# Performance work log

Hardware: AMD Instinct MI355X
Metric: run time of the kernel (lower is better)

Reference implementation:

```python
import jax, jax.numpy as jnp
import numpy as np

B, T = 32, 2000
H = 512          # hidden_size
NH = 100         # n_harmonics
NM = 65          # n_magnitudes
E = 16           # energy_state dim
HH = 256         # hypernetwork hidden


def _lin_init(k, out_d, in_d):
    return jax.random.normal(k, (out_d, in_d), jnp.float32) / np.sqrt(in_d)


def setup_inputs() -> dict:
    key = jax.random.key(0)
    ks = jax.random.split(key, 24)
    inp = {
        'f0_scaled': jax.random.uniform(ks[0], (B, T), jnp.float32),
        'loudness': jax.random.uniform(ks[1], (B, T), jnp.float32),
        'energy_state': jax.random.normal(ks[2], (B, E), jnp.float32),
        # base decoder params
        'pre_W': _lin_init(ks[3], H, 2), 'pre_b': jnp.zeros((H,), jnp.float32),
        'W_ih': _lin_init(ks[4], 3 * H, H), 'W_hh': _lin_init(ks[5], 3 * H, H),
        'b_ih': jnp.zeros((3 * H,), jnp.float32), 'b_hh': jnp.zeros((3 * H,), jnp.float32),
        'post_W': _lin_init(ks[6], H, H), 'post_b': jnp.zeros((H,), jnp.float32),
        'harm_W': _lin_init(ks[7], NH, H), 'harm_b': jnp.zeros((NH,), jnp.float32),
        'noise_W': _lin_init(ks[8], NM, H), 'noise_b': jnp.zeros((NM,), jnp.float32),
        # hypernetwork params (small output scale so deltas are perturbative)
        'hyp_W1': _lin_init(ks[9], HH, E), 'hyp_b1': jnp.zeros((HH,), jnp.float32),
        'hyp_Wdh': _lin_init(ks[10], NH * H, HH) * 0.05, 'hyp_bdh': jnp.zeros((NH * H,), jnp.float32),
        'hyp_Wbh': _lin_init(ks[11], NH, HH) * 0.05, 'hyp_bbh': jnp.zeros((NH,), jnp.float32),
        'hyp_Wdn': _lin_init(ks[12], NM * H, HH) * 0.05, 'hyp_bdn': jnp.zeros((NM * H,), jnp.float32),
        'hyp_Wbn': _lin_init(ks[13], NM, HH) * 0.05, 'hyp_bbn': jnp.zeros((NM,), jnp.float32),
    }
    return inp


def _gru(x, W_ih, W_hh, b_ih, b_hh):
    # x: [B,T,H] -> [B,T,H], torch nn.GRU cell equations
    gi = jnp.einsum('bth,gh->btg', x, W_ih) + b_ih  # [B,T,3H]
    gi = jnp.swapaxes(gi, 0, 1)  # [T,B,3H]
    h0 = jnp.zeros((x.shape[0], W_hh.shape[1]), x.dtype)

    def step(h, gi_t):
        gh = h @ W_hh.T + b_hh
        ir, iz, in_ = jnp.split(gi_t, 3, axis=-1)
        hr, hz, hn = jnp.split(gh, 3, axis=-1)
        r = jax.nn.sigmoid(ir + hr)
        z = jax.nn.sigmoid(iz + hz)
        n = jnp.tanh(in_ + r * hn)
        h_new = (1.0 - z) * n + z * h
        return h_new, h_new

    _, ys = jax.lax.scan(step, h0, gi)
    return jnp.swapaxes(ys, 0, 1)  # [B,T,H]


def reference(f0_scaled, loudness, energy_state,
              pre_W, pre_b, W_ih, W_hh, b_ih, b_hh, post_W, post_b,
              harm_W, harm_b, noise_W, noise_b,
              hyp_W1, hyp_b1, hyp_Wdh, hyp_bdh, hyp_Wbh, hyp_bbh,
              hyp_Wdn, hyp_bdn, hyp_Wbn, hyp_bbn):
    Bs = energy_state.shape[0]
    # Hypernetwork: energy_state -> per-batch weight/bias deltas
    h = jax.nn.relu(energy_state @ hyp_W1.T + hyp_b1)            # [B,HH]
    dW_harm = (h @ hyp_Wdh.T + hyp_bdh).reshape(Bs, NH, H)
    db_harm = h @ hyp_Wbh.T + hyp_bbh                            # [B,NH]
    dW_noise = (h @ hyp_Wdn.T + hyp_bdn).reshape(Bs, NM, H)
    db_noise = h @ hyp_Wbn.T + hyp_bbn                           # [B,NM]

    # Base decoder trunk
    x = jnp.stack([f0_scaled, loudness], axis=-1)                # [B,T,2]
    x = jax.nn.leaky_relu(jnp.einsum('bti,hi->bth', x, pre_W) + pre_b)
    x = _gru(x, W_ih, W_hh, b_ih, b_hh)
    x = jax.nn.leaky_relu(jnp.einsum('bth,oh->bto', x, post_W) + post_b)

    # Modulated heads: per-batch effective weight shared across T (no [B*T,O,H] blow-up)
    eff_hW = harm_W[None] + dW_harm                              # [B,NH,H]
    eff_hb = harm_b[None] + db_harm                              # [B,NH]
    harm_out = jnp.einsum('bth,boh->bto', x, eff_hW) + eff_hb[:, None, :]
    harmonic_amps = jax.nn.sigmoid(harm_out)                     # [B,T,NH]

    eff_nW = noise_W[None] + dW_noise                            # [B,NM,H]
    eff_nb = noise_b[None] + db_noise                            # [B,NM]
    noise_out = jnp.einsum('bth,boh->bto', x, eff_nW) + eff_nb[:, None, :]
    noise_mags = jax.nn.sigmoid(noise_out)                       # [B,T,NM]
    return harmonic_amps, noise_mags
```

## Files before the change

kernel.cpp:

```cpp
#include <hip/hip_runtime.h>
#include <hip/hip_fp16.h>
#include <stdint.h>

#define B_  32
#define T_  2000
#define H_  512
#define NH_ 100
#define NM_ 65

typedef _Float16 f16x8 __attribute__((ext_vector_type(8)));
typedef _Float16 f16x2 __attribute__((ext_vector_type(2)));
typedef float    f32x4 __attribute__((ext_vector_type(4)));

typedef __attribute__((address_space(3))) void lds_void_t;
typedef __attribute__((address_space(1))) void glb_void_t;

__device__ __forceinline__ void gload_lds16(const void* g, void* l) {
  __builtin_amdgcn_global_load_lds((const glb_void_t*)g, (lds_void_t*)l, 16, 0, 0);
}

__device__ __forceinline__ float sigmoidf_(float x) {
  float e = __builtin_amdgcn_exp2f(-x * 1.44269504f);
  return __builtin_amdgcn_rcpf(1.0f + e);
}
__device__ __forceinline__ float tanhf_(float x) {
  float e = __builtin_amdgcn_exp2f(x * 2.88539008f);
  return 1.0f - 2.0f * __builtin_amdgcn_rcpf(e + 1.0f);
}
__device__ __forceinline__ float dot2(unsigned w, unsigned h, float acc) {
  return __builtin_amdgcn_fdot2(__builtin_bit_cast(f16x2, w),
                                __builtin_bit_cast(f16x2, h), acc, false);
}
__device__ __forceinline__ unsigned pack2(float a, float b) {
  __half2 h = __floats2half2_rn(a, b);
  return __builtin_bit_cast(unsigned, h);
}
__device__ __forceinline__ float hsel(unsigned w, int hi) {
  __half2 h2 = __builtin_bit_cast(__half2, w);
  return hi ? __high2float(h2) : __low2float(h2);
}

__global__ void hyper1(const float* __restrict__ es, const float* __restrict__ W1,
                       const float* __restrict__ b1, float* __restrict__ hE) {
  int b = blockIdx.x, o = threadIdx.x;
  float a = b1[o];
  #pragma unroll
  for (int c = 0; c < 16; ++c) a += es[b*16 + c] * W1[o*16 + c];
  hE[b*256 + o] = fmaxf(a, 0.f);
}

__global__ void hyper2(const float* __restrict__ hE,
                       const float* __restrict__ Wbh, const float* __restrict__ bbh,
                       const float* __restrict__ harmb,
                       const float* __restrict__ Wbn, const float* __restrict__ bbn,
                       const float* __restrict__ noiseb, float* __restrict__ effb) {
  int b = blockIdx.x, o = threadIdx.x;
  if (o < NH_) {
    float a = bbh[o] + harmb[o];
    for (int c = 0; c < 256; ++c) a += hE[b*256 + c] * Wbh[o*256 + c];
    effb[b*256 + o] = a;
  } else if (o < NH_ + NM_) {
    int q = o - NH_;
    float a = bbn[q] + noiseb[q];
    for (int c = 0; c < 256; ++c) a += hE[b*256 + c] * Wbn[q*256 + c];
    effb[b*256 + o] = a;
  }
}

__global__ __launch_bounds__(256) void hyper3(
    const float* __restrict__ hE, const float* __restrict__ Wd,
    const float* __restrict__ bd, const float* __restrict__ baseW,
    __half* __restrict__ effW, int o_base) {
  __shared__ float wl[256*33];
  __shared__ float hEl[32*256];
  int tid = threadIdx.x;
  int row0 = blockIdx.x * 256;
  #pragma unroll
  for (int i = 0; i < 32; ++i) hEl[i*256 + tid] = hE[i*256 + tid];
  float acc[32];
  #pragma unroll
  for (int b = 0; b < 32; ++b) acc[b] = 0.f;
  for (int cc = 0; cc < 256; cc += 32) {
    __syncthreads();
    #pragma unroll
    for (int i = 0; i < 32; ++i) {
      int idx = i*256 + tid;
      int r = idx >> 5, c = idx & 31;
      wl[r*33 + c] = Wd[(size_t)(row0 + r)*256 + cc + c];
    }
    __syncthreads();
    #pragma unroll
    for (int c = 0; c < 32; ++c) {
      float w = wl[tid*33 + c];
      #pragma unroll
      for (int b = 0; b < 32; ++b) acc[b] += w * hEl[b*256 + cc + c];
    }
  }
  int row = row0 + tid;
  int o = row >> 9, h = row & 511;
  float base = baseW[row] + bd[row];
  #pragma unroll
  for (int b = 0; b < 32; ++b) {
    effW[((size_t)b*256 + o_base + o)*512 + h] = (__half)(acc[b] + base);
  }
}

__global__ void cvt_f16(const float* __restrict__ in, __half* __restrict__ out, int n) {
  int i = blockIdx.x*256 + threadIdx.x;
  if (i < n) out[i] = (__half)in[i];
}

__global__ void pack_whh3(const float* __restrict__ Whh, uint4* __restrict__ Wp3) {
  int idx = blockIdx.x*256 + threadIdx.x;
  int t = idx % 384;
  int k = (idx / 384) & 31;
  int w = idx / (384*32);
  int rr = t >> 1, ch = t & 1;
  int g = rr >> 6, j = rr & 63;
  int row = g*512 + w*64 + j;
  int col0 = ch*256 + k*8;
  const float* src = Whh + (size_t)row*512 + col0;
  uint4 o;
  o.x = pack2(src[0], src[1]);
  o.y = pack2(src[2], src[3]);
  o.z = pack2(src[4], src[5]);
  o.w = pack2(src[6], src[7]);
  Wp3[idx] = o;
}

__global__ void pre_kernel(const float* __restrict__ f0, const float* __restrict__ loud,
                           const float* __restrict__ preW, const float* __restrict__ preb,
                           __half* __restrict__ xpre, int CH, int c0) {
  int b = blockIdx.y;
  int idx = blockIdx.x*256 + threadIdx.x;
  int t = idx >> 9, h = idx & 511;
  int mg = b*T_ + c0 + t;
  float v = f0[mg]*preW[h*2+0] + loud[mg]*preW[h*2+1] + preb[h];
  v = v >= 0.f ? v : 0.01f*v;
  xpre[((size_t)b*CH + t)*512 + h] = (__half)v;
}

template<int ACT>
__global__ __launch_bounds__(256) void gemm_nt(
    const __half* __restrict__ A, const __half* __restrict__ B,
    __half* __restrict__ C, const float* __restrict__ bias, int N) {
  constexpr int K = 512;
  __shared__ __align__(16) __half As[128*64];
  __shared__ __align__(16) __half Bs[128*64];
  int tid = threadIdx.x;
  int bx = blockIdx.x, by = blockIdx.y;
  const __half* Ab = A + (size_t)bx*128*K;
  const __half* Bb = B + (size_t)by*128*K;
  f32x4 acc[4][4] = {};
  int lane = tid & 63;
  int wv = tid >> 6, wr = wv >> 1, wc = wv & 1;
  int lr = lane & 15, lk = lane >> 4;

  for (int kt = 0; kt < K/64; ++kt) {
    #pragma unroll
    for (int j = 0; j < 4; ++j) {
      int idx = j*256 + tid;
      int row = idx >> 3, seg = idx & 7;
      const __half* gpA = Ab + (size_t)row*K + kt*64 + seg*8;
      const __half* gpB = Bb + (size_t)row*K + kt*64 + seg*8;
      __half* lpA = As + (size_t)(j*256 + (tid & ~63))*8;
      __half* lpB = Bs + (size_t)(j*256 + (tid & ~63))*8;
      gload_lds16(gpA, lpA);
      gload_lds16(gpB, lpB);
    }
    __syncthreads();
    #pragma unroll
    for (int ks = 0; ks < 2; ++ks) {
      f16x8 af[4], bf[4];
      #pragma unroll
      for (int i = 0; i < 4; ++i)
        af[i] = *(const f16x8*)(As + (wr*64 + i*16 + lr)*64 + ks*32 + lk*8);
      #pragma unroll
      for (int j2 = 0; j2 < 4; ++j2)
        bf[j2] = *(const f16x8*)(Bs + (wc*64 + j2*16 + lr)*64 + ks*32 + lk*8);
      #pragma unroll
      for (int i = 0; i < 4; ++i)
        #pragma unroll
        for (int j2 = 0; j2 < 4; ++j2)
          acc[i][j2] = __builtin_amdgcn_mfma_f32_16x16x32_f16(af[i], bf[j2], acc[i][j2], 0, 0, 0);
    }
    __syncthreads();
  }

  #pragma unroll
  for (int j2 = 0; j2 < 4; ++j2) {
    int col = by*128 + wc*64 + j2*16 + lr;
    float bv = bias[col];
    #pragma unroll
    for (int i = 0; i < 4; ++i) {
      int row0 = bx*128 + wr*64 + i*16 + lk*4;
      #pragma unroll
      for (int r = 0; r < 4; ++r) {
        float v = acc[i][j2][r] + bv;
        if (ACT == 1) v = v >= 0.f ? v : 0.01f*v;
        C[(size_t)(row0 + r)*N + col] = (__half)v;
      }
    }
  }
}

__global__ __launch_bounds__(256) void heads_gemm(
    const __half* __restrict__ Apc, const __half* __restrict__ effW,
    const float* __restrict__ effb, float* __restrict__ out, int CH, int c0) {
  constexpr int K = 512;
  __shared__ __align__(16) __half As[128*64];
  __shared__ __align__(16) __half Bs[128*64];
  int tid = threadIdx.x;
  int bx = blockIdx.x, by = blockIdx.y, b = blockIdx.z;
  const __half* Ab = Apc + (size_t)b*CH*K;
  const __half* Bb = effW + ((size_t)b*256 + (size_t)by*128)*K;
  f32x4 acc[4][4] = {};
  int lane = tid & 63;
  int wv = tid >> 6, wr = wv >> 1, wc = wv & 1;
  int lr = lane & 15, lk = lane >> 4;

  for (int kt = 0; kt < K/64; ++kt) {
    #pragma unroll
    for (int j = 0; j < 4; ++j) {
      int idx = j*256 + tid;
      int row = idx >> 3, seg = idx & 7;
      int ar = bx*128 + row; if (ar > CH-1) ar = CH-1;
      const __half* gpA = Ab + (size_t)ar*K + kt*64 + seg*8;
      const __half* gpB = Bb + (size_t)row*K + kt*64 + seg*8;
      __half* lpA = As + (size_t)(j*256 + (tid & ~63))*8;
      __half* lpB = Bs + (size_t)(j*256 + (tid & ~63))*8;
      gload_lds16(gpA, lpA);
      gload_lds16(gpB, lpB);
    }
    __syncthreads();
    #pragma unroll
    for (int ks = 0; ks < 2; ++ks) {
      f16x8 af[4], bf[4];
      #pragma unroll
      for (int i = 0; i < 4; ++i)
        af[i] = *(const f16x8*)(As + (wr*64 + i*16 + lr)*64 + ks*32 + lk*8);
      #pragma unroll
      for (int j2 = 0; j2 < 4; ++j2)
        bf[j2] = *(const f16x8*)(Bs + (wc*64 + j2*16 + lr)*64 + ks*32 + lk*8);
      #pragma unroll
      for (int i = 0; i < 4; ++i)
        #pragma unroll
        for (int j2 = 0; j2 < 4; ++j2)
          acc[i][j2] = __builtin_amdgcn_mfma_f32_16x16x32_f16(af[i], bf[j2], acc[i][j2], 0, 0, 0);
    }
    __syncthreads();
  }

  #pragma unroll
  for (int j2 = 0; j2 < 4; ++j2) {
    int o = by*128 + wc*64 + j2*16 + lr;
    if (o < NH_ + NM_) {
      float bv = effb[b*256 + o];
      #pragma unroll
      for (int i = 0; i < 4; ++i) {
        #pragma unroll
        for (int r = 0; r < 4; ++r) {
          int trow = bx*128 + wr*64 + i*16 + lk*4 + r;
          if (trow < CH) {
            int tg = c0 + trow;
            float v = sigmoidf_(acc[i][j2][r] + bv);
            if (o < NH_)
              out[((size_t)b*T_ + tg)*NH_ + o] = v;
            else
              out[(size_t)B_*T_*NH_ + ((size_t)b*T_ + tg)*NM_ + (o - NH_)] = v;
          }
        }
      }
    }
  }
}

#define LOADW(k) { const uint4* p = Wp3 + ((size_t)(w*32 + (k)))*384 + t; \
  asm volatile("global_load_dwordx4 %0, %1, off" : "=v"(wq_##k) : "v"(p) : "memory"); }

#define DOTW(k, A) { uint4 hv = *(const uint4*)&hq[ch*132 + (k)*4]; \
  A = dot2(wq_##k.x, hv.x, A); A = dot2(wq_##k.y, hv.y, A); \
  A = dot2(wq_##k.z, hv.z, A); A = dot2(wq_##k.w, hv.w, A); }

#define BARX() do { asm volatile("s_waitcnt lgkmcnt(0)\n\ts_barrier" ::: "memory"); \
                    __builtin_amdgcn_sched_barrier(0); } while (0)

__global__ __launch_bounds__(512) __attribute__((amdgpu_waves_per_eu(2, 4)))
void gru_scan8(
    const uint4* __restrict__ Wp3, const __half* __restrict__ gi_c,
    const float* __restrict__ bhh, __half* __restrict__ ys_c,
    float* __restrict__ hstate, unsigned long long* __restrict__ xch64,
    int CH, int first) {
  int wg = blockIdx.x;
  int b = wg & 31;
  int w = wg >> 5;
  int t = threadIdx.x;
  int ch = t & 1;
  bool wact = (t < 384);
  bool comb = (t >= 384 && t < 416);
  int tc = t - 384;

  __shared__ __align__(16) unsigned hq[264];
  __shared__ float part[384];
  __shared__ float gil[192];

  uint4 wq_0{},wq_1{},wq_2{},wq_3{},wq_4{},wq_5{},wq_6{},wq_7{},
        wq_8{},wq_9{},wq_10{},wq_11{},wq_12{},wq_13{},wq_14{},wq_15{},
        wq_16{},wq_17{},wq_18{},wq_19{},wq_20{},wq_21{},wq_22{},wq_23{},
        wq_24{},wq_25{},wq_26{},wq_27{},wq_28{},wq_29{},wq_30{},wq_31{};
  if (wact) {
    LOADW(0)  LOADW(1)  LOADW(2)  LOADW(3)  LOADW(4)  LOADW(5)  LOADW(6)  LOADW(7)
    LOADW(8)  LOADW(9)  LOADW(10) LOADW(11) LOADW(12) LOADW(13) LOADW(14) LOADW(15)
    LOADW(16) LOADW(17) LOADW(18) LOADW(19) LOADW(20) LOADW(21) LOADW(22) LOADW(23)
    LOADW(24) LOADW(25) LOADW(26) LOADW(27) LOADW(28) LOADW(29) LOADW(30) LOADW(31)
  }
  asm volatile("s_waitcnt vmcnt(0)" ::: "memory");
  __builtin_amdgcn_sched_barrier(0);

  float br0=0.f,br1=0.f,bz0=0.f,bz1=0.f,bn0=0.f,bn1=0.f;
  if (comb) {
    int u0 = w*64 + 2*tc;
    br0 = bhh[u0];        br1 = bhh[u0+1];
    bz0 = bhh[512+u0];    bz1 = bhh[512+u0+1];
    bn0 = bhh[1024+u0];   bn1 = bhh[1024+u0+1];
  }

  if (t < 256) {
    unsigned hv0 = first ? 0u : pack2(hstate[b*512 + 2*t], hstate[b*512 + 2*t + 1]);
    hq[t < 128 ? t : t + 4] = hv0;
  }
  __syncthreads();

  const __half* gib = gi_c + (size_t)b*CH*1536;
  __half* ysb = ys_c + (size_t)b*CH*512;

  float giv_cur = 0.f, giv_next = 0.f;
  if (t < 192) giv_cur = (float)gib[(t >> 6)*512 + w*64 + (t & 63)];

  for (int s = 0; s < CH; ++s) {
    int p = s & 1;
    unsigned long long* xp64 = xch64 + ((size_t)p*32 + b)*256;

    if (t < 192 && s + 1 < CH)
      giv_next = (float)gib[(size_t)(s+1)*1536 + (t >> 6)*512 + w*64 + (t & 63)];

    if (wact) {
      float a0 = 0.f, a1 = 0.f, a2 = 0.f, a3 = 0.f;
      DOTW(0,a0)  DOTW(1,a1)  DOTW(2,a2)  DOTW(3,a3)
      DOTW(4,a0)  DOTW(5,a1)  DOTW(6,a2)  DOTW(7,a3)
      DOTW(8,a0)  DOTW(9,a1)  DOTW(10,a2) DOTW(11,a3)
      DOTW(12,a0) DOTW(13,a1) DOTW(14,a2) DOTW(15,a3)
      DOTW(16,a0) DOTW(17,a1) DOTW(18,a2) DOTW(19,a3)
      DOTW(20,a0) DOTW(21,a1) DOTW(22,a2) DOTW(23,a3)
      DOTW(24,a0) DOTW(25,a1) DOTW(26,a2) DOTW(27,a3)
      DOTW(28,a0) DOTW(29,a1) DOTW(30,a2) DOTW(31,a3)
      part[t] = (a0 + a1) + (a2 + a3);
      if (t < 192) gil[t] = giv_cur;
    }
    giv_cur = giv_next;
    BARX();

    if (comb) {
      int j0 = 2*tc, j1 = 2*tc + 1;
      float ghr0 = part[j0*2] + part[j0*2+1] + br0;
      float ghr1 = part[j1*2] + part[j1*2+1] + br1;
      float ghz0 = part[(64+j0)*2] + part[(64+j0)*2+1] + bz0;
      float ghz1 = part[(64+j1)*2] + part[(64+j1)*2+1] + bz1;
      float ghn0 = part[(128+j0)*2] + part[(128+j0)*2+1] + bn0;
      float ghn1 = part[(128+j1)*2] + part[(128+j1)*2+1] + bn1;
      float r0 = sigmoidf_(gil[j0] + ghr0);
      float r1 = sigmoidf_(gil[j1] + ghr1);
      float z0 = sigmoidf_(gil[64+j0] + ghz0);
      float z1 = sigmoidf_(gil[64+j1] + ghz1);
      float n0 = tanhf_(gil[128+j0] + r0*ghn0);
      float n1 = tanhf_(gil[128+j1] + r1*ghn1);
      int gidx = w*32 + tc;
      int hidx = gidx < 128 ? gidx : gidx + 4;
      unsigned hold = hq[hidx];
      float h0 = (1.f - z0)*n0 + z0*hsel(hold, 0);
      float h1 = (1.f - z1)*n1 + z1*hsel(hold, 1);
      unsigned hv = pack2(h0, h1);
      hq[hidx] = hv;
      *(unsigned*)&ysb[(size_t)s*512 + w*64 + j0] = hv;
      unsigned long long tv = ((unsigned long long)(unsigned)(s + 1) << 32)
                              | (unsigned long long)hv;
      __hip_atomic_store(&xp64[gidx], tv,
                         __ATOMIC_RELAXED, __HIP_MEMORY_SCOPE_AGENT);
      if (s == CH - 1) {
        hstate[b*512 + w*64 + j0] = h0;
        hstate[b*512 + w*64 + j1] = h1;
      }
    } else if (t < 256 && (t >> 5) != w) {
      unsigned long long v;
      do {
        v = __hip_atomic_load(&xp64[t], __ATOMIC_RELAXED, __HIP_MEMORY_SCOPE_AGENT);
      } while ((unsigned)(v >> 32) != (unsigned)(s + 1));
      hq[t < 128 ? t : t + 4] = (unsigned)v;
    }
    BARX();
  }
}

extern "C" void kernel_launch(void* const* d_in, const int* in_sizes, int n_in,
                              void* d_out, int out_size, void* d_ws, size_t ws_size,
                              hipStream_t stream) {
  const float* f0     = (const float*)d_in[0];
  const float* loud   = (const float*)d_in[1];
  const float* es     = (const float*)d_in[2];
  const float* preW   = (const float*)d_in[3];
  const float* preb   = (const float*)d_in[4];
  const float* Wih    = (const float*)d_in[5];
  const float* Whh    = (const float*)d_in[6];
  const float* b_ih   = (const float*)d_in[7];
  const float* b_hh   = (const float*)d_in[8];
  const float* postW  = (const float*)d_in[9];
  const float* postb  = (const float*)d_in[10];
  const float* harmW  = (const float*)d_in[11];
  const float* harmb  = (const float*)d_in[12];
  const float* noiseW = (const float*)d_in[13];
  const float* noiseb = (const float*)d_in[14];
  const float* hypW1  = (const float*)d_in[15];
  const float* hypb1  = (const float*)d_in[16];
  const float* Wdh    = (const float*)d_in[17];
  const float* bdh    = (const float*)d_in[18];
  const float* Wbh    = (const float*)d_in[19];
  const float* bbh    = (const float*)d_in[20];
  const float* Wdn    = (const float*)d_in[21];
  const float* bdn    = (const float*)d_in[22];
  const float* Wbn    = (const float*)d_in[23];
  const float* bbn    = (const float*)d_in[24];
  (void)in_sizes; (void)n_in; (void)out_size;

  const size_t FIXED = 13312ull*1024ull;
  int CH = 20;
  {
    const int opts[8] = {2000, 1000, 500, 400, 200, 100, 40, 20};
    for (int i = 0; i < 8; ++i) {
      size_t need = FIXED + (size_t)opts[i] * 163840ull + 65536ull;
      if (need <= ws_size) { CH = opts[i]; break; }
    }
  }
  const int NC = T_ / CH;
  const int Mc = B_ * CH;

  char* w = (char*)d_ws;
  size_t off = 0;
  auto alloc = [&](size_t bytes) -> void* {
    void* p = (void*)(w + off);
    off += (bytes + 255) & ~(size_t)255;
    return p;
  };
  float*    hE      = (float*)alloc((size_t)32*256*4);
  float*    effb    = (float*)alloc((size_t)32*256*4);
  float*    hstate  = (float*)alloc((size_t)32*512*4);
  __half*   effW    = (__half*)alloc((size_t)32*256*512*2);
  __half*   Wih16   = (__half*)alloc((size_t)1536*512*2);
  __half*   postW16 = (__half*)alloc((size_t)512*512*2);
  uint4*    Wp3     = (uint4*)alloc((size_t)8*32*384*16 + 4096);
  unsigned long long* xch64 = (unsigned long long*)alloc((size_t)2*32*256*8);
  __half*   xpre    = (__half*)alloc((size_t)Mc*512*2);
  __half*   gibuf   = (__half*)alloc((size_t)Mc*1536*2);
  __half*   ysbuf   = (__half*)alloc((size_t)Mc*512*2);
  __half*   postc   = xpre;

  hyper1<<<32, 256, 0, stream>>>(es, hypW1, hypb1, hE);
  hyper2<<<32, 256, 0, stream>>>(hE, Wbh, bbh, harmb, Wbn, bbn, noiseb, effb);
  hyper3<<<200, 256, 0, stream>>>(hE, Wdh, bdh, harmW, effW, 0);
  hyper3<<<130, 256, 0, stream>>>(hE, Wdn, bdn, noiseW, effW, NH_);
  cvt_f16<<<(1536*512)/256, 256, 0, stream>>>(Wih, Wih16, 1536*512);
  cvt_f16<<<(512*512)/256, 256, 0, stream>>>(postW, postW16, 512*512);
  pack_whh3<<<384, 256, 0, stream>>>(Whh, Wp3);

  for (int c = 0; c < NC; ++c) {
    int c0 = c * CH;
    pre_kernel<<<dim3(CH*2, 32), 256, 0, stream>>>(f0, loud, preW, preb, xpre, CH, c0);
    gemm_nt<0><<<dim3(Mc/128, 12), 256, 0, stream>>>(xpre, Wih16, gibuf, b_ih, 1536);
    gru_scan8<<<256, 512, 0, stream>>>(Wp3, gibuf, b_hh, ysbuf, hstate, xch64,
                                       CH, c == 0 ? 1 : 0);
    gemm_nt<1><<<dim3(Mc/128, 4), 256, 0, stream>>>(ysbuf, postW16, postc, postb, 512);
    heads_gemm<<<dim3((CH+127)/128, 2, 32), 256, 0, stream>>>(postc, effW, effb,
                                                              (float*)d_out, CH, c0);
  }
}
```

Measured before the change: 4.630 ms.

## Repartition GRU recurrent matvec so each thread reuses 8 h vectors across 4 rows

After: 4.267 ms (median of 2 runs). 1.09x faster.

```diff
diff --git a/kernel.cpp b/kernel.cpp
--- a/kernel.cpp
+++ b/kernel.cpp
@@ -38,6 +38,10 @@
 __device__ __forceinline__ float hsel(unsigned w, int hi) {
   __half2 h2 = __builtin_bit_cast(__half2, w);
   return hi ? __high2float(h2) : __low2float(h2);
+}
+__device__ __forceinline__ int hq_swz(int i) {
+  int cs = i >> 5, kk = (i >> 2) & 7;
+  return cs*32 + ((kk ^ cs) << 2) + (i & 3);
 }
 
 __global__ void hyper1(const float* __restrict__ es, const float* __restrict__ W1,
@@ -110,22 +114,22 @@
   if (i < n) out[i] = (__half)in[i];
 }
 
-__global__ void pack_whh3(const float* __restrict__ Whh, uint4* __restrict__ Wp3) {
+__global__ void pack_whh4(const float* __restrict__ Whh, uint4* __restrict__ Wp) {
   int idx = blockIdx.x*256 + threadIdx.x;
   int t = idx % 384;
   int k = (idx / 384) & 31;
   int w = idx / (384*32);
-  int rr = t >> 1, ch = t & 1;
-  int g = rr >> 6, j = rr & 63;
-  int row = g*512 + w*64 + j;
-  int col0 = ch*256 + k*8;
+  int rq = t >> 3, cs = t & 7;
+  int j = k >> 3, kk = k & 7;
+  int row = (rq >> 4)*512 + w*64 + (rq & 15)*4 + j;
+  int col0 = cs*64 + kk*8;
   const float* src = Whh + (size_t)row*512 + col0;
   uint4 o;
   o.x = pack2(src[0], src[1]);
   o.y = pack2(src[2], src[3]);
   o.z = pack2(src[4], src[5]);
   o.w = pack2(src[6], src[7]);
-  Wp3[idx] = o;
+  Wp[idx] = o;
 }
 
 __global__ void pre_kernel(const float* __restrict__ f0, const float* __restrict__ loud,
@@ -275,10 +279,10 @@
   }
 }
 
-#define LOADW(k) { const uint4* p = Wp3 + ((size_t)(w*32 + (k)))*384 + t; \
+#define LOADW(k) { const uint4* p = Wp + ((size_t)(w*32 + (k)))*384 + t; \
   asm volatile("global_load_dwordx4 %0, %1, off" : "=v"(wq_##k) : "v"(p) : "memory"); }
 
-#define DOTW(k, A) { uint4 hv = *(const uint4*)&hq[ch*132 + (k)*4]; \
+#define DOT4(k, hv, A) { \
   A = dot2(wq_##k.x, hv.x, A); A = dot2(wq_##k.y, hv.y, A); \
   A = dot2(wq_##k.z, hv.z, A); A = dot2(wq_##k.w, hv.w, A); }
 
@@ -287,7 +291,7 @@
 
 __global__ __launch_bounds__(512) __attribute__((amdgpu_waves_per_eu(2, 4)))
 void gru_scan8(
-    const uint4* __restrict__ Wp3, const __half* __restrict__ gi_c,
+    const uint4* __restrict__ Wp, const __half* __restrict__ gi_c,
     const float* __restrict__ bhh, __half* __restrict__ ys_c,
     float* __restrict__ hstate, unsigned long long* __restrict__ xch64,
     int CH, int first) {
@@ -295,13 +299,13 @@
   int b = wg & 31;
   int w = wg >> 5;
   int t = threadIdx.x;
-  int ch = t & 1;
+  int rq = t >> 3, cs = t & 7;
   bool wact = (t < 384);
   bool comb = (t >= 384 && t < 416);
   int tc = t - 384;
 
-  __shared__ __align__(16) unsigned hq[264];
-  __shared__ float part[384];
+  __shared__ __align__(16) unsigned hq[256];
+  __shared__ float part[192];
   __shared__ float gil[192];
 
   uint4 wq_0{},wq_1{},wq_2{},wq_3{},wq_4{},wq_5{},wq_6{},wq_7{},
@@ -327,12 +331,14 @@
 
   if (t < 256) {
     unsigned hv0 = first ? 0u : pack2(hstate[b*512 + 2*t], hstate[b*512 + 2*t + 1]);
-    hq[t < 128 ? t : t + 4] = hv0;
+    hq[hq_swz(t)] = hv0;
   }
   __syncthreads();
 
   const __half* gib = gi_c + (size_t)b*CH*1536;
   __half* ysb = ys_c + (size_t)b*CH*512;
+  const uint4* hq4 = (const uint4*)hq;
+  int hb = cs*8;
 
   float giv_cur = 0.f, giv_next = 0.f;
   if (t < 192) giv_cur = (float)gib[(t >> 6)*512 + w*64 + (t & 63)];
@@ -345,16 +351,31 @@
       giv_next = (float)gib[(size_t)(s+1)*1536 + (t >> 6)*512 + w*64 + (t & 63)];
 
     if (wact) {
+      uint4 hv0_ = hq4[hb + (0 ^ cs)];
+      uint4 hv1_ = hq4[hb + (1 ^ cs)];
+      uint4 hv2_ = hq4[hb + (2 ^ cs)];
+      uint4 hv3_ = hq4[hb + (3 ^ cs)];
+      uint4 hv4_ = hq4[hb + (4 ^ cs)];
+      uint4 hv5_ = hq4[hb + (5 ^ cs)];
+      uint4 hv6_ = hq4[hb + (6 ^ cs)];
+      uint4 hv7_ = hq4[hb + (7 ^ cs)];
       float a0 = 0.f, a1 = 0.f, a2 = 0.f, a3 = 0.f;
-      DOTW(0,a0)  DOTW(1,a1)  DOTW(2,a2)  DOTW(3,a3)
-      DOTW(4,a0)  DOTW(5,a1)  DOTW(6,a2)  DOTW(7,a3)
-      DOTW(8,a0)  DOTW(9,a1)  DOTW(10,a2) DOTW(11,a3)
-      DOTW(12,a0) DOTW(13,a1) DOTW(14,a2) DOTW(15,a3)
-      DOTW(16,a0) DOTW(17,a1) DOTW(18,a2) DOTW(19,a3)
-      DOTW(20,a0) DOTW(21,a1) DOTW(22,a2) DOTW(23,a3)
-      DOTW(24,a0) DOTW(25,a1) DOTW(26,a2) DOTW(27,a3)
-      DOTW(28,a0) DOTW(29,a1) DOTW(30,a2) DOTW(31,a3)
-      part[t] = (a0 + a1) + (a2 + a3);
+      DOT4(0,hv0_,a0)  DOT4(8,hv0_,a1)  DOT4(16,hv0_,a2) DOT4(24,hv0_,a3)
+      DOT4(1,hv1_,a0)  DOT4(9,hv1_,a1)  DOT4(17,hv1_,a2) DOT4(25,hv1_,a3)
+      DOT4(2,hv2_,a0)  DOT4(10,hv2_,a1) DOT4(18,hv2_,a2) DOT4(26,hv2_,a3)
+      DOT4(3,hv3_,a0)  DOT4(11,hv3_,a1) DOT4(19,hv3_,a2) DOT4(27,hv3_,a3)
+      DOT4(4,hv4_,a0)  DOT4(12,hv4_,a1) DOT4(20,hv4_,a2) DOT4(28,hv4_,a3)
+      DOT4(5,hv5_,a0)  DOT4(13,hv5_,a1) DOT4(21,hv5_,a2) DOT4(29,hv5_,a3)
+      DOT4(6,hv6_,a0)  DOT4(14,hv6_,a1) DOT4(22,hv6_,a2) DOT4(30,hv6_,a3)
+      DOT4(7,hv7_,a0)  DOT4(15,hv7_,a1) DOT4(23,hv7_,a2) DOT4(31,hv7_,a3)
+      a0 += __shfl_xor(a0, 1); a0 += __shfl_xor(a0, 2); a0 += __shfl_xor(a0, 4);
+      a1 += __shfl_xor(a1, 1); a1 += __shfl_xor(a1, 2); a1 += __shfl_xor(a1, 4);
+      a2 += __shfl_xor(a2, 1); a2 += __shfl_xor(a2, 2); a2 += __shfl_xor(a2, 4);
+      a3 += __shfl_xor(a3, 1); a3 += __shfl_xor(a3, 2); a3 += __shfl_xor(a3, 4);
+      if (cs < 4) {
+        float v = (cs == 0) ? a0 : (cs == 1) ? a1 : (cs == 2) ? a2 : a3;
+        part[(rq << 2) + cs] = v;
+      }
       if (t < 192) gil[t] = giv_cur;
     }
     giv_cur = giv_next;
@@ -362,20 +383,14 @@
 
     if (comb) {
       int j0 = 2*tc, j1 = 2*tc + 1;
-      float ghr0 = part[j0*2] + part[j0*2+1] + br0;
-      float ghr1 = part[j1*2] + part[j1*2+1] + br1;
-      float ghz0 = part[(64+j0)*2] + part[(64+j0)*2+1] + bz0;
-      float ghz1 = part[(64+j1)*2] + part[(64+j1)*2+1] + bz1;
-      float ghn0 = part[(128+j0)*2] + part[(128+j0)*2+1] + bn0;
-      float ghn1 = part[(128+j1)*2] + part[(128+j1)*2+1] + bn1;
-      float r0 = sigmoidf_(gil[j0] + ghr0);
-      float r1 = sigmoidf_(gil[j1] + ghr1);
-      float z0 = sigmoidf_(gil[64+j0] + ghz0);
-      float z1 = sigmoidf_(gil[64+j1] + ghz1);
-      float n0 = tanhf_(gil[128+j0] + r0*ghn0);
-      float n1 = tanhf_(gil[128+j1] + r1*ghn1);
+      float r0 = sigmoidf_(gil[j0] + part[j0] + br0);
+      float r1 = sigmoidf_(gil[j1] + part[j1] + br1);
+      float z0 = sigmoidf_(gil[64+j0] + part[64+j0] + bz0);
+      float z1 = sigmoidf_(gil[64+j1] + part[64+j1] + bz1);
+      float n0 = tanhf_(gil[128+j0] + r0*(part[128+j0] + bn0));
+      float n1 = tanhf_(gil[128+j1] + r1*(part[128+j1] + bn1));
       int gidx = w*32 + tc;
-      int hidx = gidx < 128 ? gidx : gidx + 4;
+      int hidx = hq_swz(gidx);
       unsigned hold = hq[hidx];
       float h0 = (1.f - z0)*n0 + z0*hsel(hold, 0);
       float h1 = (1.f - z1)*n1 + z1*hsel(hold, 1);
@@ -395,7 +410,7 @@
       do {
         v = __hip_atomic_load(&xp64[t], __ATOMIC_RELAXED, __HIP_MEMORY_SCOPE_AGENT);
       } while ((unsigned)(v >> 32) != (unsigned)(s + 1));
-      hq[t < 128 ? t : t + 4] = (unsigned)v;
+      hq[hq_swz(t)] = (unsigned)v;
     }
     BARX();
   }
@@ -456,7 +471,7 @@
   __half*   effW    = (__half*)alloc((size_t)32*256*512*2);
   __half*   Wih16   = (__half*)alloc((size_t)1536*512*2);
   __half*   postW16 = (__half*)alloc((size_t)512*512*2);
-  uint4*    Wp3     = (uint4*)alloc((size_t)8*32*384*16 + 4096);
+  uint4*    Wp      = (uint4*)alloc((size_t)8*32*384*16 + 4096);
   unsigned long long* xch64 = (unsigned long long*)alloc((size_t)2*32*256*8);
   __half*   xpre    = (__half*)alloc((size_t)Mc*512*2);
   __half*   gibuf   = (__half*)alloc((size_t)Mc*1536*2);
@@ -469,13 +484,13 @@
   hyper3<<<130, 256, 0, stream>>>(hE, Wdn, bdn, noiseW, effW, NH_);
   cvt_f16<<<(1536*512)/256, 256, 0, stream>>>(Wih, Wih16, 1536*512);
   cvt_f16<<<(512*512)/256, 256, 0, stream>>>(postW, postW16, 512*512);
-  pack_whh3<<<384, 256, 0, stream>>>(Whh, Wp3);
+  pack_whh4<<<384, 256, 0, stream>>>(Whh, Wp);
 
   for (int c = 0; c < NC; ++c) {
     int c0 = c * CH;
     pre_kernel<<<dim3(CH*2, 32), 256, 0, stream>>>(f0, loud, preW, preb, xpre, CH, c0);
     gemm_nt<0><<<dim3(Mc/128, 12), 256, 0, stream>>>(xpre, Wih16, gibuf, b_ih, 1536);
-    gru_scan8<<<256, 512, 0, stream>>>(Wp3, gibuf, b_hh, ysbuf, hstate, xch64,
+    gru_scan8<<<256, 512, 0, stream>>>(Wp, gibuf, b_hh, ysbuf, hstate, xch64,
                                        CH, c == 0 ? 1 : 0);
     gemm_nt<1><<<dim3(Mc/128, 4), 256, 0, stream>>>(ysbuf, postW16, postc, postb, 512);
     heads_gemm<<<dim3((CH+127)/128, 2, 32), 256, 0, stream>>>(postc, effW, effb,
```

## Restructure GRU scan to one barrier per step with DPP reductions

Applied to the files above, without the earlier changes.

Measured after the change: 5.407 ms. 1.17x slower.

```diff
diff --git a/kernel.cpp b/kernel.cpp
--- a/kernel.cpp
+++ b/kernel.cpp
@@ -35,9 +35,9 @@
   __half2 h = __floats2half2_rn(a, b);
   return __builtin_bit_cast(unsigned, h);
 }
-__device__ __forceinline__ float hsel(unsigned w, int hi) {
-  __half2 h2 = __builtin_bit_cast(__half2, w);
-  return hi ? __high2float(h2) : __low2float(h2);
+__device__ __forceinline__ int wslot(int i) {
+  int q = i >> 5;
+  return (q << 5) + (((((i >> 2) & 7) ^ q)) << 2) + (i & 3);
 }
 
 __global__ void hyper1(const float* __restrict__ es, const float* __restrict__ W1,
@@ -110,22 +110,22 @@
   if (i < n) out[i] = (__half)in[i];
 }
 
-__global__ void pack_whh3(const float* __restrict__ Whh, uint4* __restrict__ Wp3) {
+__global__ void pack_whh5(const float* __restrict__ Whh, uint4* __restrict__ Wp) {
   int idx = blockIdx.x*256 + threadIdx.x;
-  int t = idx % 384;
-  int k = (idx / 384) & 31;
-  int w = idx / (384*32);
-  int rr = t >> 1, ch = t & 1;
-  int g = rr >> 6, j = rr & 63;
-  int row = g*512 + w*64 + j;
-  int col0 = ch*256 + k*8;
+  int t = idx & 511;
+  int k = (idx >> 9) % 24;
+  int w = idx / (512*24);
+  int g = k >> 3, kk = k & 7;
+  int u = t >> 3, cs = t & 7;
+  int row = g*512 + w*64 + u;
+  int col0 = cs*64 + kk*8;
   const float* src = Whh + (size_t)row*512 + col0;
   uint4 o;
   o.x = pack2(src[0], src[1]);
   o.y = pack2(src[2], src[3]);
   o.z = pack2(src[4], src[5]);
   o.w = pack2(src[6], src[7]);
-  Wp3[idx] = o;
+  Wp[idx] = o;
 }
 
 __global__ void pre_kernel(const float* __restrict__ f0, const float* __restrict__ loud,
@@ -275,19 +275,24 @@
   }
 }
 
-#define LOADW(k) { const uint4* p = Wp3 + ((size_t)(w*32 + (k)))*384 + t; \
-  asm volatile("global_load_dwordx4 %0, %1, off" : "=v"(wq_##k) : "v"(p) : "memory"); }
-
-#define DOTW(k, A) { uint4 hv = *(const uint4*)&hq[ch*132 + (k)*4]; \
-  A = dot2(wq_##k.x, hv.x, A); A = dot2(wq_##k.y, hv.y, A); \
-  A = dot2(wq_##k.z, hv.z, A); A = dot2(wq_##k.w, hv.w, A); }
+#define LOADW(k) { const uint4* p_ = Wp + ((size_t)(w*24 + (k)))*512 + t; \
+  asm volatile("global_load_dwordx4 %0, %1, off" : "=v"(wq_##k) : "v"(p_) : "memory"); }
+
+#define DOTU(W, hv, A) { A = dot2(W.x, hv.x, A); A = dot2(W.y, hv.y, A); \
+                         A = dot2(W.z, hv.z, A); A = dot2(W.w, hv.w, A); }
+
+#define GS(kr, kz, kn, kk) { uint4 hv = hq4[(cs << 3) + ((kk) ^ cs)]; \
+  DOTU(wq_##kr, hv, ar) DOTU(wq_##kz, hv, az) DOTU(wq_##kn, hv, an) }
+
+#define DPPADD(a, ctrl) ((a) + __builtin_bit_cast(float, \
+  __builtin_amdgcn_update_dpp(0, __builtin_bit_cast(int, (a)), (ctrl), 0xF, 0xF, true)))
 
 #define BARX() do { asm volatile("s_waitcnt lgkmcnt(0)\n\ts_barrier" ::: "memory"); \
                     __builtin_amdgcn_sched_barrier(0); } while (0)
 
 __global__ __launch_bounds__(512) __attribute__((amdgpu_waves_per_eu(2, 4)))
-void gru_scan8(
-    const uint4* __restrict__ Wp3, const __half* __restrict__ gi_c,
+void gru_scan9(
+    const uint4* __restrict__ Wp, const __half* __restrict__ gi_c,
     const float* __restrict__ bhh, __half* __restrict__ ys_c,
     float* __restrict__ hstate, unsigned long long* __restrict__ xch64,
     int CH, int first) {
@@ -295,107 +300,85 @@
   int b = wg & 31;
   int w = wg >> 5;
   int t = threadIdx.x;
-  int ch = t & 1;
-  bool wact = (t < 384);
-  bool comb = (t >= 384 && t < 416);
-  int tc = t - 384;
-
-  __shared__ __align__(16) unsigned hq[264];
-  __shared__ float part[384];
-  __shared__ float gil[192];
+  int u = t >> 3, cs = t & 7;
+
+  __shared__ __align__(16) unsigned hq[2][264];
 
   uint4 wq_0{},wq_1{},wq_2{},wq_3{},wq_4{},wq_5{},wq_6{},wq_7{},
         wq_8{},wq_9{},wq_10{},wq_11{},wq_12{},wq_13{},wq_14{},wq_15{},
-        wq_16{},wq_17{},wq_18{},wq_19{},wq_20{},wq_21{},wq_22{},wq_23{},
-        wq_24{},wq_25{},wq_26{},wq_27{},wq_28{},wq_29{},wq_30{},wq_31{};
-  if (wact) {
-    LOADW(0)  LOADW(1)  LOADW(2)  LOADW(3)  LOADW(4)  LOADW(5)  LOADW(6)  LOADW(7)
-    LOADW(8)  LOADW(9)  LOADW(10) LOADW(11) LOADW(12) LOADW(13) LOADW(14) LOADW(15)
-    LOADW(16) LOADW(17) LOADW(18) LOADW(19) LOADW(20) LOADW(21) LOADW(22) LOADW(23)
-    LOADW(24) LOADW(25) LOADW(26) LOADW(27) LOADW(28) LOADW(29) LOADW(30) LOADW(31)
-  }
+        wq_16{},wq_17{},wq_18{},wq_19{},wq_20{},wq_21{},wq_22{},wq_23{};
+  LOADW(0)  LOADW(1)  LOADW(2)  LOADW(3)  LOADW(4)  LOADW(5)  LOADW(6)  LOADW(7)
+  LOADW(8)  LOADW(9)  LOADW(10) LOADW(11) LOADW(12) LOADW(13) LOADW(14) LOADW(15)
+  LOADW(16) LOADW(17) LOADW(18) LOADW(19) LOADW(20) LOADW(21) LOADW(22) LOADW(23)
   asm volatile("s_waitcnt vmcnt(0)" ::: "memory");
   __builtin_amdgcn_sched_barrier(0);
 
-  float br0=0.f,br1=0.f,bz0=0.f,bz1=0.f,bn0=0.f,bn1=0.f;
-  if (comb) {
-    int u0 = w*64 + 2*tc;
-    br0 = bhh[u0];        br1 = bhh[u0+1];
-    bz0 = bhh[512+u0];    bz1 = bhh[512+u0+1];
-    bn0 = bhh[1024+u0];   bn1 = bhh[1024+u0+1];
-  }
-
+  int ug = w*64 + u;
+  float br = 0.f, bz = 0.f, bn = 0.f, hreg = 0.f;
+  if (cs == 0) {
+    br = bhh[ug]; bz = bhh[512 + ug]; bn = bhh[1024 + ug];
+    hreg = first ? 0.f : hstate[b*512 + ug];
+  }
   if (t < 256) {
     unsigned hv0 = first ? 0u : pack2(hstate[b*512 + 2*t], hstate[b*512 + 2*t + 1]);
-    hq[t < 128 ? t : t + 4] = hv0;
+    hq[0][wslot(t)] = hv0;
   }
   __syncthreads();
 
   const __half* gib = gi_c + (size_t)b*CH*1536;
   __half* ysb = ys_c + (size_t)b*CH*512;
 
-  float giv_cur = 0.f, giv_next = 0.f;
-  if (t < 192) giv_cur = (float)gib[(t >> 6)*512 + w*64 + (t & 63)];
+  float gr_c = 0.f, gz_c = 0.f, gn_c = 0.f, gr_n = 0.f, gz_n = 0.f, gn_n = 0.f;
+  if (cs == 0) {
+    gr_c = (float)gib[ug]; gz_c = (float)gib[512 + ug]; gn_c = (float)gib[1024 + ug];
+  }
 
   for (int s = 0; s < CH; ++s) {
     int p = s & 1;
     unsigned long long* xp64 = xch64 + ((size_t)p*32 + b)*256;
 
-    if (t < 192 && s + 1 < CH)
-      giv_next = (float)gib[(size_t)(s+1)*1536 + (t >> 6)*512 + w*64 + (t & 63)];
-
-    if (wact) {
-      float a0 = 0.f, a1 = 0.f, a2 = 0.f, a3 = 0.f;
-      DOTW(0,a0)  DOTW(1,a1)  DOTW(2,a2)  DOTW(3,a3)
-      DOTW(4,a0)  DOTW(5,a1)  DOTW(6,a2)  DOTW(7,a3)
-      DOTW(8,a0)  DOTW(9,a1)  DOTW(10,a2) DOTW(11,a3)
-      DOTW(12,a0) DOTW(13,a1) DOTW(14,a2) DOTW(15,a3)
-      DOTW(16,a0) DOTW(17,a1) DOTW(18,a2) DOTW(19,a3)
-      DOTW(20,a0) DOTW(21,a1) DOTW(22,a2) DOTW(23,a3)
-      DOTW(24,a0) DOTW(25,a1) DOTW(26,a2) DOTW(27,a3)
-      DOTW(28,a0) DOTW(29,a1) DOTW(30,a2) DOTW(31,a3)
-      part[t] = (a0 + a1) + (a2 + a3);
-      if (t < 192) gil[t] = giv_cur;
-    }
-    giv_cur = giv_next;
-    BARX();
-
-    if (comb) {
-      int j0 = 2*tc, j1 = 2*tc + 1;
-      float ghr0 = part[j0*2] + part[j0*2+1] + br0;
-      float ghr1 = part[j1*2] + part[j1*2+1] + br1;
-      float ghz0 = part[(64+j0)*2] + part[(64+j0)*2+1] + bz0;
-      float ghz1 = part[(64+j1)*2] + part[(64+j1)*2+1] + bz1;
-      float ghn0 = part[(128+j0)*2] + part[(128+j0)*2+1] + bn0;
-      float ghn1 = part[(128+j1)*2] + part[(128+j1)*2+1] + bn1;
-      float r0 = sigmoidf_(gil[j0] + ghr0);
-      float r1 = sigmoidf_(gil[j1] + ghr1);
-      float z0 = sigmoidf_(gil[64+j0] + ghz0);
-      float z1 = sigmoidf_(gil[64+j1] + ghz1);
-      float n0 = tanhf_(gil[128+j0] + r0*ghn0);
-      float n1 = tanhf_(gil[128+j1] + r1*ghn1);
-      int gidx = w*32 + tc;
-      int hidx = gidx < 128 ? gidx : gidx + 4;
-      unsigned hold = hq[hidx];
-      float h0 = (1.f - z0)*n0 + z0*hsel(hold, 0);
-      float h1 = (1.f - z1)*n1 + z1*hsel(hold, 1);
-      unsigned hv = pack2(h0, h1);
-      hq[hidx] = hv;
-      *(unsigned*)&ysb[(size_t)s*512 + w*64 + j0] = hv;
-      unsigned long long tv = ((unsigned long long)(unsigned)(s + 1) << 32)
-                              | (unsigned long long)hv;
-      __hip_atomic_store(&xp64[gidx], tv,
-                         __ATOMIC_RELAXED, __HIP_MEMORY_SCOPE_AGENT);
-      if (s == CH - 1) {
-        hstate[b*512 + w*64 + j0] = h0;
-        hstate[b*512 + w*64 + j1] = h1;
+    if (cs == 0 && s + 1 < CH) {
+      const __half* g1 = gib + (size_t)(s + 1)*1536 + ug;
+      gr_n = (float)g1[0]; gz_n = (float)g1[512]; gn_n = (float)g1[1024];
+    }
+
+    const uint4* hq4 = (const uint4*)&hq[p][0];
+    float ar = 0.f, az = 0.f, an = 0.f;
+    GS(0,8,16,0)  GS(1,9,17,1)  GS(2,10,18,2)  GS(3,11,19,3)
+    GS(4,12,20,4) GS(5,13,21,5) GS(6,14,22,6)  GS(7,15,23,7)
+
+    ar = DPPADD(ar, 0xB1); ar = DPPADD(ar, 0x4E); ar = DPPADD(ar, 0x141);
+    az = DPPADD(az, 0xB1); az = DPPADD(az, 0x4E); az = DPPADD(az, 0x141);
+    an = DPPADD(an, 0xB1); an = DPPADD(an, 0x4E); an = DPPADD(an, 0x141);
+
+    if (cs == 0) {
+      float r = sigmoidf_(gr_c + ar + br);
+      float z = sigmoidf_(gz_c + az + bz);
+      float n = tanhf_(gn_c + r*(an + bn));
+      float h = (1.f - z)*n + z*hreg;
+      hreg = h;
+      unsigned myh = pack2(h, 0.f);
+      unsigned oth = (unsigned)__builtin_amdgcn_update_dpp(
+          0, (int)myh, 0x128, 0xF, 0xF, true);
+      if (!(u & 1)) {
+        unsigned hv = (oth << 16) | myh;
+        int pi = (w << 5) + (u >> 1);
+        hq[p ^ 1][wslot(pi)] = hv;
+        *(unsigned*)&ysb[(size_t)s*512 + ug] = hv;
+        unsigned long long tv = ((unsigned long long)(unsigned)(s + 1) << 32)
+                                | (unsigned long long)hv;
+        __hip_atomic_store(&xp64[pi], tv,
+                           __ATOMIC_RELAXED, __HIP_MEMORY_SCOPE_AGENT);
       }
-    } else if (t < 256 && (t >> 5) != w) {
+      if (s == CH - 1) hstate[b*512 + ug] = h;
+      gr_c = gr_n; gz_c = gz_n; gn_c = gn_n;
+    }
+    if (t < 256 && (t >> 5) != w) {
       unsigned long long v;
       do {
         v = __hip_atomic_load(&xp64[t], __ATOMIC_RELAXED, __HIP_MEMORY_SCOPE_AGENT);
       } while ((unsigned)(v >> 32) != (unsigned)(s + 1));
-      hq[t < 128 ? t : t + 4] = (unsigned)v;
+      hq[p ^ 1][wslot(t)] = (unsigned)v;
     }
     BARX();
   }
@@ -456,7 +439,7 @@
   __half*   effW    = (__half*)alloc((size_t)32*256*512*2);
   __half*   Wih16   = (__half*)alloc((size_t)1536*512*2);
   __half*   postW16 = (__half*)alloc((size_t)512*512*2);
-  uint4*    Wp3     = (uint4*)alloc((size_t)8*32*384*16 + 4096);
+  uint4*    Wp      = (uint4*)alloc((size_t)8*24*512*16 + 4096);
   unsigned long long* xch64 = (unsigned long long*)alloc((size_t)2*32*256*8);
   __half*   xpre    = (__half*)alloc((size_t)Mc*512*2);
   __half*   gibuf   = (__half*)alloc((size_t)Mc*1536*2);
@@ -469,13 +452,13 @@
   hyper3<<<130, 256, 0, stream>>>(hE, Wdn, bdn, noiseW, effW, NH_);
   cvt_f16<<<(1536*512)/256, 256, 0, stream>>>(Wih, Wih16, 1536*512);
   cvt_f16<<<(512*512)/256, 256, 0, stream>>>(postW, postW16, 512*512);
-  pack_whh3<<<384, 256, 0, stream>>>(Whh, Wp3);
+  pack_whh5<<<384, 256, 0, stream>>>(Whh, Wp);
 
   for (int c = 0; c < NC; ++c) {
     int c0 = c * CH;
     pre_kernel<<<dim3(CH*2, 32), 256, 0, stream>>>(f0, loud, preW, preb, xpre, CH, c0);
     gemm_nt<0><<<dim3(Mc/128, 12), 256, 0, stream>>>(xpre, Wih16, gibuf, b_ih, 1536);
-    gru_scan8<<<256, 512, 0, stream>>>(Wp3, gibuf, b_hh, ysbuf, hstate, xch64,
+    gru_scan9<<<256, 512, 0, stream>>>(Wp, gibuf, b_hh, ysbuf, hstate, xch64,
                                        CH, c == 0 ? 1 : 0);
     gemm_nt<1><<<dim3(Mc/128, 4), 256, 0, stream>>>(ysbuf, postW16, postc, postb, 512);
     heads_gemm<<<dim3((CH+127)/128, 2, 32), 256, 0, stream>>>(postc, effW, effb,
```
